# Performance work log

Hardware: AMD Instinct MI355X
Metric: run time of the kernel (lower is better)

## Reference

```python
import jax, jax.numpy as jnp
import numpy as np

BLUR = 0.05
P = 2
EPS_FINAL = BLUR ** P          # geomloss: eps = blur**p = 0.0025
DIAMETER = 2.0                 # max cosine cost magnitude
SCALING = 0.5                  # geomloss default; eps decays by scaling**p per step
N_FINAL_ITERS = 4              # extra balancing iterations at the final eps


def eps_schedule():
    eps_list = []
    e = DIAMETER ** P
    while e > EPS_FINAL:
        eps_list.append(e)
        e = e * (SCALING ** P)
    eps_list.extend([EPS_FINAL] * N_FINAL_ITERS)
    return eps_list


def cosine_cost(a, b):
    # a: (N, D), b: (M, D) -> (N, M) cost = 1 - cos_sim
    an = a / (jnp.linalg.norm(a, axis=1, keepdims=True) + 1e-12)
    bn = b / (jnp.linalg.norm(b, axis=1, keepdims=True) + 1e-12)
    return 1.0 - an @ bn.T


def softmin(C, pot, log_w, eps):
    # -eps * LSE_j( log_w + (pot_j - C_ij)/eps ) ; C: (N, M), pot: (M,)
    return -eps * jax.nn.logsumexp(log_w + (pot[None, :] - C) / eps, axis=1)


def sinkhorn_divergence(Cxy, Cxx, Cyy):
    N, M = Cxy.shape
    log_a = -jnp.log(jnp.asarray(N, dtype=Cxy.dtype))  # uniform weights
    log_b = -jnp.log(jnp.asarray(M, dtype=Cxy.dtype))
    sg = jax.lax.stop_gradient
    # Sinkhorn iterations run on detached costs (geomloss envelope-theorem trick)
    Cxy_s, Cxx_s, Cyy_s = sg(Cxy), sg(Cxx), sg(Cyy)
    f = jnp.zeros((N,), Cxy.dtype)
    g = jnp.zeros((M,), Cxy.dtype)
    fxx = jnp.zeros((N,), Cxy.dtype)
    gyy = jnp.zeros((M,), Cxy.dtype)
    for eps in eps_schedule():
        # symmetric (debiasing) potentials: averaged fixed-point update
        fxx = 0.5 * (fxx + softmin(Cxx_s, fxx, log_a, eps))
        gyy = 0.5 * (gyy + softmin(Cyy_s, gyy, log_b, eps))
        # cross potentials: simultaneous (Jacobi) update
        f, g = softmin(Cxy_s, g, log_b, eps), softmin(Cxy_s.T, f, log_a, eps)
    # final extrapolation step with gradients flowing through the costs
    eps = EPS_FINAL
    f_fin = softmin(Cxy, sg(g), log_b, eps)
    g_fin = softmin(Cxy.T, sg(f), log_a, eps)
    fxx_fin = softmin(Cxx, sg(fxx), log_a, eps)
    gyy_fin = softmin(Cyy, sg(gyy), log_b, eps)
    return jnp.mean(f_fin - fxx_fin) + jnp.mean(g_fin - gyy_fin)


def setup_inputs() -> dict:
    key = jax.random.key(0)
    k1, k2, k3 = jax.random.split(key, 3)
    x1 = jax.random.normal(k1, (8192, 256), dtype=jnp.float32)
    x2 = jax.random.normal(k2, (8192, 256), dtype=jnp.float32)
    w = jax.random.uniform(k3, (256,), dtype=jnp.float32)
    return {"x1": x1, "x2": x2, "w": w}


def reference(x1, x2, w):
    # Dist_loss.forward: clamp+renormalize learned per-feature weights, scale x1
    w_c = jnp.clip(w, 0.0, 2.0)
    w_c = w_c / jnp.mean(w_c)
    a = w_c[None, :] * x1
    Cxy = cosine_cost(a, x2)
    Cxx = cosine_cost(a, a)
    Cyy = cosine_cost(x2, x2)
    return sinkhorn_divergence(Cxy, Cxx, Cyy)
```

## Files before the change

kernel.cpp:

```cpp
#include <hip/hip_runtime.h>
#include <math.h>

#define N 8192
#define D 256
#define LN2 0.6931471805599453f

typedef short short8 __attribute__((ext_vector_type(8)));
typedef float f32x16 __attribute__((ext_vector_type(16)));
typedef unsigned short ushort;

__device__ __forceinline__ float fexp2(float x) { return __builtin_amdgcn_exp2f(x); }
__device__ __forceinline__ float flog2(float x) { return __builtin_amdgcn_logf(x); }

__device__ __forceinline__ ushort bf16r(float x) {
    unsigned int u = __float_as_uint(x);
    return (ushort)((u + 0x7FFF + ((u >> 16) & 1)) >> 16);
}

__global__ void prep_wc(const float* __restrict__ w, float* __restrict__ wc) {
    int t = threadIdx.x;
    float v = fminf(fmaxf(w[t], 0.0f), 2.0f);
    float s = v;
#pragma unroll
    for (int m = 1; m < 64; m <<= 1) s += __shfl_xor(s, m);
    __shared__ float sm[4];
    if ((t & 63) == 0) sm[t >> 6] = s;
    __syncthreads();
    float mean = (sm[0] + sm[1] + sm[2] + sm[3]) * (1.0f / 256.0f);
    wc[t] = v / mean;
}

__global__ void prep_normalize(const float* __restrict__ x1, const float* __restrict__ x2,
                               const float* __restrict__ wc,
                               ushort* __restrict__ an_t, ushort* __restrict__ bn_t) {
    int row = blockIdx.x;
    int t = threadIdx.x;
    int r; float v; ushort* ip;
    if (row < N) { r = row;     v = x1[(size_t)r * D + t] * wc[t]; ip = an_t; }
    else         { r = row - N; v = x2[(size_t)r * D + t];         ip = bn_t; }
    float ss = v * v;
#pragma unroll
    for (int m = 1; m < 64; m <<= 1) ss += __shfl_xor(ss, m);
    __shared__ float sm[4];
    if ((t & 63) == 0) sm[t >> 6] = ss;
    __syncthreads();
    float denom = sqrtf(sm[0] + sm[1] + sm[2] + sm[3]) + 1e-12f;
    __shared__ __attribute__((aligned(16))) ushort ls[256];
    ls[t] = bf16r(v / denom);
    __syncthreads();
    if (t < 32) {
        int c = t >> 1, lh = t & 1;
        short8 vv = *(const short8*)&ls[c * 16 + lh * 8];
        size_t base = (size_t)(r >> 5) * 8192 + (size_t)c * 512 + lh * 256 + (r & 31) * 8;
        *(short8*)(ip + base) = vv;
    }
}

__global__ void init_pots(float* __restrict__ pots, float* __restrict__ potm1) {
    int id = blockIdx.x * 256 + threadIdx.x;
    pots[id] = 0.0f;
    potm1[id] = -1.0f;
}

__global__ __launch_bounds__(256, 2) void softmin_mfma(
    const ushort* __restrict__ an_t, const ushort* __restrict__ bn_t,
    const float* __restrict__ potm1,
    float2* __restrict__ parts, float k1) {
    int bx = blockIdx.x;
    int k = bx & 7;
    int q = bx >> 3;
    int task = k >> 1;
    int split = ((k & 1) << 1) | (q & 1);
    int rb = q >> 1;
    const ushort* jp = (task == 0 || task == 3) ? an_t : bn_t;
    const ushort* ip = (task == 0 || task == 2) ? an_t : bn_t;
    const float* pm1 = potm1 + (size_t)task * N;

    int t = threadIdx.x;
    int wave = t >> 6, lane = t & 63;
    int l31 = lane & 31, lh = lane >> 5;
    int i0 = rb * 256 + wave * 64;

    short8 bi0[16], bi1[16];
    {
        const ushort* ib = ip + (size_t)(i0 >> 5) * 8192 + lane * 8;
#pragma unroll
        for (int c = 0; c < 16; ++c) {
            bi0[c] = *(const short8*)(ib + c * 512);
            bi1[c] = *(const short8*)(ib + 8192 + c * 512);
        }
    }
#pragma unroll
    for (int c = 0; c < 16; ++c) {
        asm volatile("" : "+a"(bi0[c]), "+a"(bi1[c]));
    }

    const int jbase0 = split * 2048;
    const ushort* ab = jp + (size_t)(jbase0 >> 5) * 8192 + lane * 8;
    const float*  pb = pm1 + jbase0 + 4 * lh;

    f32x16 c0, c1;
    short8 af[16];

    auto ldaf = [&]() {
#pragma unroll
        for (int c = 0; c < 16; ++c)
            af[c] = *(const short8*)(ab + c * 512);
    };
    auto ldpot = [&]() {
        float4 p0 = *(const float4*)(pb + 0);
        float4 p1 = *(const float4*)(pb + 8);
        float4 p2 = *(const float4*)(pb + 16);
        float4 p3 = *(const float4*)(pb + 24);
        c0[0] = p0.x; c0[1] = p0.y; c0[2]  = p0.z; c0[3]  = p0.w;
        c0[4] = p1.x; c0[5] = p1.y; c0[6]  = p1.z; c0[7]  = p1.w;
        c0[8] = p2.x; c0[9] = p2.y; c0[10] = p2.z; c0[11] = p2.w;
        c0[12] = p3.x; c0[13] = p3.y; c0[14] = p3.z; c0[15] = p3.w;
        c1 = c0;
    };

    float m0 = -INFINITY, s0 = 0.0f, m1 = -INFINITY, s1 = 0.0f;

    auto lse = [&](const f32x16& c, float& m, float& s) {
        float g0 = fmaxf(fmaxf(c[0],  c[1]),  c[2]);
        float g1 = fmaxf(fmaxf(c[3],  c[4]),  c[5]);
        float g2 = fmaxf(fmaxf(c[6],  c[7]),  c[8]);
        float g3 = fmaxf(fmaxf(c[9],  c[10]), c[11]);
        float g4 = fmaxf(fmaxf(c[12], c[13]), c[14]);
        float h  = fmaxf(fmaxf(g0, g1), g2);
        float mx = fmaxf(fmaxf(h, g3), fmaxf(g4, c[15]));
        float mn = fmaxf(m, mx * k1);
        float nm = -mn;
        float t0 = fexp2(fmaf(c[0],  k1, nm)) + fexp2(fmaf(c[1],  k1, nm));
        float t1 = fexp2(fmaf(c[2],  k1, nm)) + fexp2(fmaf(c[3],  k1, nm));
        float t2 = fexp2(fmaf(c[4],  k1, nm)) + fexp2(fmaf(c[5],  k1, nm));
        float t3 = fexp2(fmaf(c[6],  k1, nm)) + fexp2(fmaf(c[7],  k1, nm));
        float t4 = fexp2(fmaf(c[8],  k1, nm)) + fexp2(fmaf(c[9],  k1, nm));
        float t5 = fexp2(fmaf(c[10], k1, nm)) + fexp2(fmaf(c[11], k1, nm));
        float t6 = fexp2(fmaf(c[12], k1, nm)) + fexp2(fmaf(c[13], k1, nm));
        float t7 = fexp2(fmaf(c[14], k1, nm)) + fexp2(fmaf(c[15], k1, nm));
        float ad = ((t0 + t1) + (t2 + t3)) + ((t4 + t5) + (t6 + t7));
        s = fmaf(s, fexp2(m - mn), ad);
        m = mn;
    };

    ldpot();
    ldaf();
    for (int js = 0; js < 64; ++js) {
        __builtin_amdgcn_s_setprio(1);
#pragma unroll
        for (int c = 0; c < 16; ++c) {
            short8 a = af[c];
            c0 = __builtin_amdgcn_mfma_f32_32x32x16_bf16(a, bi0[c], c0, 0, 0, 0);
            c1 = __builtin_amdgcn_mfma_f32_32x32x16_bf16(a, bi1[c], c1, 0, 0, 0);
        }
        __builtin_amdgcn_s_setprio(0);
        ab += 8192;
        if (js < 63) ldaf();
        lse(c0, m0, s0);
        lse(c1, m1, s1);
        pb += 32;
        if (js < 63) ldpot();
    }

    float mo = __shfl_xor(m0, 32), so = __shfl_xor(s0, 32);
    float M0 = fmaxf(m0, mo);
    float S0 = s0 * fexp2(m0 - M0) + so * fexp2(mo - M0);
    mo = __shfl_xor(m1, 32); so = __shfl_xor(s1, 32);
    float M1 = fmaxf(m1, mo);
    float S1 = s1 * fexp2(m1 - M1) + so * fexp2(mo - M1);
    if (lane < 32) {
        size_t r0 = (size_t)task * N + (i0 + l31);
        size_t r1 = r0 + 32;
        parts[r0 * 4 + split] = make_float2(M0, S0);
        parts[r1 * 4 + split] = make_float2(M1, S1);
    }
}

__global__ void merge_pots(const float2* __restrict__ parts, float* __restrict__ pots,
                           float* __restrict__ potm1, float eps, float logw, int do_avg) {
    int id = blockIdx.x * 256 + threadIdx.x;
    int task = id >> 13;
    int row = id & (N - 1);
    const float2* p = parts + (size_t)id * 4;
    float2 a = p[0], b = p[1], c = p[2], d = p[3];
    float M = fmaxf(fmaxf(a.x, b.x), fmaxf(c.x, d.x));
    float S = a.y * fexp2(a.x - M) + b.y * fexp2(b.x - M) +
              c.y * fexp2(c.x - M) + d.y * fexp2(d.x - M);
    float lse = LN2 * (M + flog2(S));
    float v = -eps * (logw + lse);
    if (do_avg && task < 2) v = 0.5f * (pots[id] + v);
    pots[id] = v;
    int ct = (task < 2) ? task : (5 - task);
    potm1[(size_t)ct * N + row] = v - 1.0f;
}

__global__ void final_reduce(const float* __restrict__ pots, float* __restrict__ out) {
    int t = threadIdx.x;
    float s = 0.0f;
    for (int i = t; i < N; i += 256)
        s += (pots[2 * N + i] - pots[i]) + (pots[3 * N + i] - pots[N + i]);
#pragma unroll
    for (int m = 1; m < 64; m <<= 1) s += __shfl_xor(s, m);
    __shared__ float sm[4];
    if ((t & 63) == 0) sm[t >> 6] = s;
    __syncthreads();
    if (t == 0) out[0] = (sm[0] + sm[1] + sm[2] + sm[3]) * (1.0f / (float)N);
}

extern "C" void kernel_launch(void* const* d_in, const int* in_sizes, int n_in,
                              void* d_out, int out_size, void* d_ws, size_t ws_size,
                              hipStream_t stream) {
    const float* x1 = (const float*)d_in[0];
    const float* x2 = (const float*)d_in[1];
    const float* w  = (const float*)d_in[2];
    float* out = (float*)d_out;

    ushort* an_t = (ushort*)d_ws;
    ushort* bn_t = an_t + (size_t)N * D;
    float*  wc   = (float*)(bn_t + (size_t)N * D);
    float*  pots = wc + 256;
    float*  potm1 = pots + 4 * N;
    float2* parts = (float2*)(potm1 + 4 * N);

    prep_wc<<<1, 256, 0, stream>>>(w, wc);
    prep_normalize<<<2 * N, 256, 0, stream>>>(x1, x2, wc, an_t, bn_t);
    init_pots<<<4 * N / 256, 256, 0, stream>>>(pots, potm1);

    const float eps_list[10] = {4.0f, 1.0f, 0.25f, 0.0625f, 0.015625f,
                                0.00390625f, 0.0025f, 0.0025f, 0.0025f, 0.0025f};
    const float logw = -logf((float)N);
    const float LOG2E = 1.4426950408889634f;
    for (int it = 0; it < 10; ++it) {
        softmin_mfma<<<512, 256, 0, stream>>>(an_t, bn_t, potm1, parts, LOG2E / eps_list[it]);
        merge_pots<<<4 * N / 256, 256, 0, stream>>>(parts, pots, potm1,
                                                    eps_list[it], logw, 1);
    }
    softmin_mfma<<<512, 256, 0, stream>>>(an_t, bn_t, potm1, parts, LOG2E / 0.0025f);
    merge_pots<<<4 * N / 256, 256, 0, stream>>>(parts, pots, potm1, 0.0025f, logw, 0);
    final_reduce<<<1, 256, 0, stream>>>(pots, out);
}
```

Before: 1.793 ms.

## Double-buffer MFMA accumulators to overlap softmin LSE with next tile's matmul

Splits the accumulators into two sets (a0/a1, b0/b1) and software-pipelines the loop so the MFMA chain for tile j+1 is issued while the exp/logsumexp for tile j runs. It adds sched_group_barrier hints that interleave one MFMA with four VALU ops, so the transcendental work hides under matrix-core latency. The aim is to remove the serialization between matmul and the exp-heavy reduction. The cost is 32 extra accumulator registers, which raises register pressure and may lower occupancy or cause spills. The potential loads are also duplicated into both buffers instead of being copied.

Measured after the change: 3.975 ms. 122% more time.

```diff
diff --git a/kernel.cpp b/kernel.cpp
--- a/kernel.cpp
+++ b/kernel.cpp
@@ -96,18 +96,20 @@
     }
 
     const int jbase0 = split * 2048;
-    const ushort* ab = jp + (size_t)(jbase0 >> 5) * 8192 + lane * 8;
-    const float*  pb = pm1 + jbase0 + 4 * lh;
-
-    f32x16 c0, c1;
+    const ushort* abp = jp + (size_t)(jbase0 >> 5) * 8192 + lane * 8;
+    const float*  pbp = pm1 + jbase0 + 4 * lh;
+
+    f32x16 a0, a1, b0, b1;
     short8 af[16];
 
-    auto ldaf = [&]() {
+    auto ldaf = [&](int js) {
+        const ushort* ab = abp + (size_t)js * 8192;
 #pragma unroll
         for (int c = 0; c < 16; ++c)
             af[c] = *(const short8*)(ab + c * 512);
     };
-    auto ldpot = [&]() {
+    auto ldpot = [&](int js, f32x16& c0, f32x16& c1) {
+        const float* pb = pbp + js * 32;
         float4 p0 = *(const float4*)(pb + 0);
         float4 p1 = *(const float4*)(pb + 8);
         float4 p2 = *(const float4*)(pb + 16);
@@ -116,7 +118,22 @@
         c0[4] = p1.x; c0[5] = p1.y; c0[6]  = p1.z; c0[7]  = p1.w;
         c0[8] = p2.x; c0[9] = p2.y; c0[10] = p2.z; c0[11] = p2.w;
         c0[12] = p3.x; c0[13] = p3.y; c0[14] = p3.z; c0[15] = p3.w;
-        c1 = c0;
+        float4 q0 = *(const float4*)(pb + 0);
+        float4 q1 = *(const float4*)(pb + 8);
+        float4 q2 = *(const float4*)(pb + 16);
+        float4 q3 = *(const float4*)(pb + 24);
+        c1[0] = q0.x; c1[1] = q0.y; c1[2]  = q0.z; c1[3]  = q0.w;
+        c1[4] = q1.x; c1[5] = q1.y; c1[6]  = q1.z; c1[7]  = q1.w;
+        c1[8] = q2.x; c1[9] = q2.y; c1[10] = q2.z; c1[11] = q2.w;
+        c1[12] = q3.x; c1[13] = q3.y; c1[14] = q3.z; c1[15] = q3.w;
+    };
+    auto chain = [&](f32x16& c0, f32x16& c1) {
+#pragma unroll
+        for (int c = 0; c < 16; ++c) {
+            short8 a = af[c];
+            c0 = __builtin_amdgcn_mfma_f32_32x32x16_bf16(a, bi0[c], c0, 0, 0, 0);
+            c1 = __builtin_amdgcn_mfma_f32_32x32x16_bf16(a, bi1[c], c1, 0, 0, 0);
+        }
     };
 
     float m0 = -INFINITY, s0 = 0.0f, m1 = -INFINITY, s1 = 0.0f;
@@ -144,24 +161,39 @@
         m = mn;
     };
 
-    ldpot();
-    ldaf();
-    for (int js = 0; js < 64; ++js) {
-        __builtin_amdgcn_s_setprio(1);
-#pragma unroll
-        for (int c = 0; c < 16; ++c) {
-            short8 a = af[c];
-            c0 = __builtin_amdgcn_mfma_f32_32x32x16_bf16(a, bi0[c], c0, 0, 0, 0);
-            c1 = __builtin_amdgcn_mfma_f32_32x32x16_bf16(a, bi1[c], c1, 0, 0, 0);
+    auto sgb = [&]() {
+#pragma unroll
+        for (int g = 0; g < 32; ++g) {
+            __builtin_amdgcn_sched_group_barrier(0x008, 1, 0);
+            __builtin_amdgcn_sched_group_barrier(0x002, 4, 0);
         }
-        __builtin_amdgcn_s_setprio(0);
-        ab += 8192;
-        if (js < 63) ldaf();
-        lse(c0, m0, s0);
-        lse(c1, m1, s1);
-        pb += 32;
-        if (js < 63) ldpot();
-    }
+    };
+
+    ldpot(0, a0, a1);
+    ldaf(0);
+    chain(a0, a1);
+    ldpot(1, b0, b1);
+    ldaf(1);
+    for (int k2 = 0; k2 < 31; ++k2) {
+        chain(b0, b1);
+        lse(a0, m0, s0);
+        lse(a1, m1, s1);
+        ldpot(2 * k2 + 2, a0, a1);
+        ldaf(2 * k2 + 2);
+        sgb();
+        chain(a0, a1);
+        lse(b0, m0, s0);
+        lse(b1, m1, s1);
+        ldpot(2 * k2 + 3, b0, b1);
+        ldaf(2 * k2 + 3);
+        sgb();
+    }
+    chain(b0, b1);
+    lse(a0, m0, s0);
+    lse(a1, m1, s1);
+    sgb();
+    lse(b0, m0, s0);
+    lse(b1, m1, s1);
 
     float mo = __shfl_xor(m0, 32), so = __shfl_xor(s0, 32);
     float M0 = fmaxf(m0, mo);
```
